# Kernel optimization log

Measured on AMD Instinct MI355X. Metric: run time of the kernel, lower is better.

Reference implementation:

```python
import jax, jax.numpy as jnp
import numpy as np
import math

B, S, E, H = 4, 1024, 1024, 16
DK = E // H  # 64


def setup_inputs() -> dict:
    key = jax.random.key(0)
    ks = jax.random.split(key, 10)
    sc = 0.02
    inp = {
        "x": jax.random.normal(ks[0], (B, S, E), dtype=jnp.float32),
        "mask": jax.random.randint(ks[1], (B, S, S), 0, 2, dtype=jnp.int32),
        "Wq": jax.random.normal(ks[2], (E, E), dtype=jnp.float32) * sc,
        "bq": jnp.zeros((E,), dtype=jnp.float32),
        "Wk": jax.random.normal(ks[3], (E, E), dtype=jnp.float32) * sc,
        "bk": jnp.zeros((E,), dtype=jnp.float32),
        "Wv": jax.random.normal(ks[4], (E, E), dtype=jnp.float32) * sc,
        "bv": jnp.zeros((E,), dtype=jnp.float32),
        "Wo": jax.random.normal(ks[5], (E, E), dtype=jnp.float32) * sc,
        "bo": jnp.zeros((E,), dtype=jnp.float32),
    }
    return inp


def _split_heads(t):
    # [B, S, E] -> [B, H, S, DK]
    return t.reshape(B, S, H, DK).transpose(0, 2, 1, 3)


def reference(x, mask, Wq, bq, Wk, bk, Wv, bv, Wo, bo):
    # Linear projections (torch Linear: y = x @ W.T + b)
    q = _split_heads(x @ Wq.T + bq)
    k = _split_heads(x @ Wk.T + bk)
    v = _split_heads(x @ Wv.T + bv)  # computed but discarded, faithful to source bug
    # scores: [B, H, S, S]
    scores = jnp.einsum('bhqd,bhkd->bhqk', q, k) / jnp.float32(math.sqrt(DK))
    scores = jnp.where(mask[:, None, :, :] == 0, jnp.float32(-1e9), scores)
    scores = jax.nn.softmax(scores, axis=-1)
    # NOTE: source forward keeps dropout(scores) (eval mode -> identity) and
    # DISCARDS matmul(scores, v). We replicate that exactly.
    attn = scores  # [B, H, S, S]
    attn = attn.transpose(0, 2, 1, 3).reshape(B, -1, E)  # [B, S*S/DK, E]
    return attn @ Wo.T + bo
```

## Files before the change

kernel.cpp:

```cpp
#include <hip/hip_runtime.h>

typedef __bf16 bf16;
typedef __attribute__((ext_vector_type(8))) __bf16 bf16x8;
typedef __attribute__((ext_vector_type(4))) float f32x4;


__device__ __forceinline__ unsigned short f2bf(float f) {
    union { float f; unsigned u; } v; v.f = f;
    unsigned r = v.u + 0x7FFFu + ((v.u >> 16) & 1u);
    return (unsigned short)(r >> 16);
}

__device__ __forceinline__ void stage128x64(const bf16* g, int ld_elems,
                                            bf16* lds, int tid) {
    const char* gb = (const char*)g;
    const int ldb = ld_elems * 2;
#pragma unroll
    for (int r = 0; r < 4; ++r) {
        int lin = r * 256 + tid;
        int row = lin >> 3;
        int ch  = (lin & 7) ^ (row & 7);
        __builtin_amdgcn_global_load_lds(
            (const __attribute__((address_space(1))) void*)(gb + (size_t)row * ldb + ch * 16),
            (__attribute__((address_space(3))) void*)(lds + lin * 8),
            16, 0, 0);
    }
}

__device__ __forceinline__ void stage_half512(const bf16* g, bf16* lds, int tid) {
    const char* gb = (const char*)g;
#pragma unroll
    for (int r = 0; r < 2; ++r) {
        int lin = r * 512 + tid;
        int row = lin >> 3;
        int ch  = (lin & 7) ^ (row & 7);
        __builtin_amdgcn_global_load_lds(
            (const __attribute__((address_space(1))) void*)(gb + (size_t)row * 2048 + ch * 16),
            (__attribute__((address_space(3))) void*)(lds + lin * 8),
            16, 0, 0);
    }
}

__device__ __forceinline__ void mma_tile(const bf16* As, const bf16* Bs,
                                         int wm, int wn, int lane,
                                         f32x4 acc[4][4]) {
    const int lm = lane & 15;
    const int g  = lane >> 4;
#pragma unroll
    for (int ks = 0; ks < 2; ++ks) {
        const int c = ks * 4 + g;
        bf16x8 a[4], b[4];
#pragma unroll
        for (int t = 0; t < 4; ++t) {
            const int row = wm * 64 + t * 16 + lm;
            a[t] = *(const bf16x8*)(As + row * 64 + ((c ^ (row & 7)) << 3));
        }
#pragma unroll
        for (int t = 0; t < 4; ++t) {
            const int row = wn * 64 + t * 16 + lm;
            b[t] = *(const bf16x8*)(Bs + row * 64 + ((c ^ (row & 7)) << 3));
        }
#pragma unroll
        for (int i = 0; i < 4; ++i)
#pragma unroll
            for (int j = 0; j < 4; ++j)
                acc[i][j] = __builtin_amdgcn_mfma_f32_16x16x32_bf16(a[i], b[j], acc[i][j], 0, 0, 0);
    }
}


__global__ void convert_kernel(const float* __restrict__ x,  const float* __restrict__ Wq,
                               const float* __restrict__ Wk, const float* __restrict__ Wo,
                               unsigned short* xb, unsigned short* Wqb,
                               unsigned short* Wkb, unsigned short* Wob) {
    size_t i = ((size_t)blockIdx.x * 256 + threadIdx.x) * 4;
    const float* src; unsigned short* dst; size_t off;
    if      (i < 4194304) { src = x;  dst = xb;  off = i; }
    else if (i < 5242880) { src = Wq; dst = Wqb; off = i - 4194304; }
    else if (i < 6291456) { src = Wk; dst = Wkb; off = i - 5242880; }
    else                  { src = Wo; dst = Wob; off = i - 6291456; }
    float4 v = *(const float4*)(src + off);
    ushort4 o;
    o.x = f2bf(v.x); o.y = f2bf(v.y); o.z = f2bf(v.z); o.w = f2bf(v.w);
    *(ushort4*)(dst + off) = o;
}

__global__ __launch_bounds__(256) void proj_kernel(
        const bf16* __restrict__ X, const bf16* __restrict__ Wqb,
        const bf16* __restrict__ Wkb, const float* __restrict__ bq,
        const float* __restrict__ bk, unsigned short* Qb, unsigned short* Kb) {
    __shared__ bf16 As[128 * 64];
    __shared__ bf16 Bs[128 * 64];
    const int tid = threadIdx.x, wid = tid >> 6, lane = tid & 63;
    const int wm = wid >> 1, wn = wid & 1;
    const int n0 = blockIdx.x * 128, m0 = blockIdx.y * 128;
    const bf16*  W    = blockIdx.z ? Wkb : Wqb;
    const float* bias = blockIdx.z ? bk  : bq;
    unsigned short* Out = blockIdx.z ? Kb : Qb;

    f32x4 acc[4][4];
    const f32x4 z4 = {0.f, 0.f, 0.f, 0.f};
#pragma unroll
    for (int i = 0; i < 4; ++i)
#pragma unroll
        for (int j = 0; j < 4; ++j) acc[i][j] = z4;

    for (int kt = 0; kt < 16; ++kt) {
        stage128x64(X + (size_t)m0 * 1024 + kt * 64, 1024, As, tid);
        stage128x64(W + (size_t)n0 * 1024 + kt * 64, 1024, Bs, tid);
        __syncthreads();
        mma_tile(As, Bs, wm, wn, lane, acc);
        __syncthreads();
    }

    const int q = lane >> 4, lm = lane & 15;
#pragma unroll
    for (int j = 0; j < 4; ++j) {
        const int col = n0 + wn * 64 + j * 16 + lm;
        const float bc = bias[col];
#pragma unroll
        for (int i = 0; i < 4; ++i)
#pragma unroll
            for (int r = 0; r < 4; ++r) {
                const int row = m0 + wm * 64 + i * 16 + q * 4 + r;
                Out[(size_t)row * 1024 + col] = f2bf(acc[i][j][r] + bc);
            }
    }
}

__global__ __launch_bounds__(256) void scores_kernel(
        const bf16* __restrict__ Qb, const bf16* __restrict__ Kb,
        const int* __restrict__ mask, unsigned short* Pun, float* Z) {
    __shared__ bf16 As[128 * 64];
    __shared__ bf16 Bs[2][128 * 64];
    __shared__ float Zs[2][128];
    const int tid = threadIdx.x, wid = tid >> 6, lane = tid & 63;
    const int wm = wid >> 1, wn = wid & 1;
    const int i0 = blockIdx.x * 128;
    const int h = blockIdx.y & 15, b = blockIdx.y >> 4;
    const int q = lane >> 4, lm = lane & 15;

    const bf16* Qh = Qb + ((size_t)(b * 1024 + i0)) * 1024 + h * 64;
    const bf16* Kh = Kb + ((size_t)(b * 1024)) * 1024 + h * 64;

    stage128x64(Qh, 1024, As, tid);
    stage128x64(Kh, 1024, Bs[0], tid);

    float rs[4][4];
#pragma unroll
    for (int i = 0; i < 4; ++i)
#pragma unroll
        for (int r = 0; r < 4; ++r) rs[i][r] = 0.f;

    for (int jt = 0; jt < 8; ++jt) {
        __syncthreads();
        if (jt < 7)
            stage128x64(Kh + (size_t)(jt + 1) * 128 * 1024, 1024, Bs[(jt + 1) & 1], tid);

        f32x4 acc[4][4];
        const f32x4 z4 = {0.f, 0.f, 0.f, 0.f};
#pragma unroll
        for (int i = 0; i < 4; ++i)
#pragma unroll
            for (int j = 0; j < 4; ++j) acc[i][j] = z4;
        mma_tile(As, Bs[jt & 1], wm, wn, lane, acc);

#pragma unroll
        for (int i = 0; i < 4; ++i)
#pragma unroll
            for (int r = 0; r < 4; ++r) {
                const int ii = i0 + wm * 64 + i * 16 + q * 4 + r;
                const size_t mrow = (size_t)b * 16384 + (size_t)ii * 16 + h;
#pragma unroll
                for (int j = 0; j < 4; ++j) {
                    const int jj = jt * 128 + wn * 64 + j * 16 + lm;
                    const float s = acc[i][j][r] * 0.125f;
                    const int mk = mask[((size_t)b * 1024 + ii) * 1024 + jj];
                    const float p = mk ? __expf(s) : 0.f;
                    Pun[mrow * 1024 + jj] = f2bf(p);
                    rs[i][r] += p;
                }
            }
    }

#pragma unroll
    for (int i = 0; i < 4; ++i)
#pragma unroll
        for (int r = 0; r < 4; ++r) {
            float v = rs[i][r];
            for (int off = 1; off < 16; off <<= 1) v += __shfl_xor(v, off, 16);
            if (lm == 0) Zs[wn][wm * 64 + i * 16 + q * 4 + r] = v;
        }
    __syncthreads();
    if (tid < 128) {
        const size_t m = (size_t)b * 16384 + (size_t)(i0 + tid) * 16 + h;
        Z[m] = Zs[0][tid] + Zs[1][tid];
    }
}

__global__ __launch_bounds__(512, 2) void out_gemm_kernel(
        const bf16* __restrict__ Pun, const bf16* __restrict__ Wob,
        const float* __restrict__ Z, const float* __restrict__ bo,
        float* __restrict__ out) {
    __shared__ bf16 As[2][2][128 * 64];
    __shared__ bf16 Bs[2][2][128 * 64];
    const int tid = threadIdx.x, wid = tid >> 6, lane = tid & 63;
    const int wm = wid >> 2, wn = wid & 3;
    const int lm = lane & 15, g = lane >> 4;

    const int bx = blockIdx.x, xcd = bx & 7, j = bx >> 3;
    const int m0 = (xcd * 32 + (j >> 2)) * 256;
    const int n0 = (j & 3) * 256;
    const bf16* Apan = Pun + (size_t)m0 * 1024;
    const bf16* Bpan = Wob + (size_t)n0 * 1024;

    f32x4 acc[8][4];
    const f32x4 z4 = {0.f, 0.f, 0.f, 0.f};
#pragma unroll
    for (int mi = 0; mi < 8; ++mi)
#pragma unroll
        for (int nj = 0; nj < 4; ++nj) acc[mi][nj] = z4;

    stage_half512(Bpan,                   Bs[0][0], tid);
    stage_half512(Bpan + 128 * 1024,      Bs[0][1], tid);
    stage_half512(Apan,                   As[0][0], tid);
    stage_half512(Apan + 128 * 1024,      As[0][1], tid);
    stage_half512(Bpan + 64,              Bs[1][0], tid);
    stage_half512(Bpan + 128 * 1024 + 64, Bs[1][1], tid);
    stage_half512(Apan + 64,              As[1][0], tid);
    asm volatile("s_waitcnt vmcnt(6)" ::: "memory");
    __builtin_amdgcn_s_barrier();
    __builtin_amdgcn_sched_barrier(0);

    bf16x8 b[8];

#define MFMA16(MH, KS)                                                        \
    _Pragma("unroll")                                                         \
    for (int mi = 0; mi < 4; ++mi)                                            \
      _Pragma("unroll")                                                       \
      for (int nj = 0; nj < 4; ++nj)                                          \
        acc[(MH) * 4 + mi][nj] = __builtin_amdgcn_mfma_f32_16x16x32_bf16(     \
            a[mi], b[(KS) * 4 + nj], acc[(MH) * 4 + mi][nj], 0, 0, 0);

#define PHASE(BUF, MH, KS, RB, STAGE, GATE)                                   \
  {                                                                           \
    const bf16* pA = &As[BUF][wm][((MH) * 64 + lm) * 64];                     \
    const int csk = (((KS) * 4 + g) ^ (lm & 7)) << 3;                         \
    bf16x8 a[4];                                                              \
    _Pragma("unroll")                                                         \
    for (int mi = 0; mi < 4; ++mi)                                            \
      a[mi] = *(const bf16x8*)(pA + mi * 16 * 64 + csk);                      \
    if (RB) {                                                                 \
      const bf16* pB = &Bs[BUF][wn >> 1][((wn & 1) * 64 + lm) * 64];          \
      _Pragma("unroll")                                                       \
      for (int k2 = 0; k2 < 2; ++k2) {                                        \
        const int cs2 = ((k2 * 4 + g) ^ (lm & 7)) << 3;                       \
        _Pragma("unroll")                                                     \
        for (int nj = 0; nj < 4; ++nj)                                        \
          b[k2 * 4 + nj] = *(const bf16x8*)(pB + nj * 16 * 64 + cs2);         \
      }                                                                       \
    }                                                                         \
    STAGE;                                                                    \
    __builtin_amdgcn_s_barrier();                                             \
    asm volatile("s_waitcnt lgkmcnt(0)" ::: "memory");                        \
    __builtin_amdgcn_sched_barrier(0);                                        \
    __builtin_amdgcn_s_setprio(1);                                            \
    MFMA16(MH, KS);                                                           \
    __builtin_amdgcn_s_setprio(0);                                            \
    __builtin_amdgcn_sched_barrier(0);                                        \
    GATE;                                                                     \
    __builtin_amdgcn_s_barrier();                                             \
    __builtin_amdgcn_sched_barrier(0);                                        \
  }

#pragma unroll 1
    for (int t = 0; t < 16; t += 2) {
        const bool more = (t < 14);
        PHASE(0, 0, 0, true,
              stage_half512(Apan + 128 * 1024 + (t + 1) * 64, As[1][1], tid), )
        PHASE(0, 1, 0, false,
              if (more) { stage_half512(Bpan + (t + 2) * 64, Bs[0][0], tid);
                          stage_half512(Bpan + 128 * 1024 + (t + 2) * 64, Bs[0][1], tid); }, )
        PHASE(0, 0, 1, false, , )
        PHASE(0, 1, 1, false,
              if (more) stage_half512(Apan + (t + 2) * 64, As[0][0], tid),
              if (more) { asm volatile("s_waitcnt vmcnt(6)" ::: "memory"); }
              else      { asm volatile("s_waitcnt vmcnt(0)" ::: "memory"); } )
        PHASE(1, 0, 0, true,
              if (more) stage_half512(Apan + 128 * 1024 + (t + 2) * 64, As[0][1], tid), )
        PHASE(1, 1, 0, false,
              if (more) { stage_half512(Bpan + (t + 3) * 64, Bs[1][0], tid);
                          stage_half512(Bpan + 128 * 1024 + (t + 3) * 64, Bs[1][1], tid); }, )
        PHASE(1, 0, 1, false, , )
        PHASE(1, 1, 1, false,
              if (more) stage_half512(Apan + (t + 3) * 64, As[1][0], tid),
              if (more) { asm volatile("s_waitcnt vmcnt(6)" ::: "memory"); } )
    }
#undef PHASE
#undef MFMA16

#pragma unroll
    for (int mi = 0; mi < 8; ++mi) {
#pragma unroll
        for (int r = 0; r < 4; ++r) {
            const int row = m0 + wm * 128 + mi * 16 + g * 4 + r;
            const float zi = 1.0f / Z[row];
#pragma unroll
            for (int nj = 0; nj < 4; ++nj) {
                const int col = n0 + wn * 64 + nj * 16 + lm;
                out[(size_t)row * 1024 + col] = acc[mi][nj][r] * zi + bo[col];
            }
        }
    }
}


extern "C" void kernel_launch(void* const* d_in, const int* in_sizes, int n_in,
                              void* d_out, int out_size, void* d_ws, size_t ws_size,
                              hipStream_t stream) {
    (void)in_sizes; (void)n_in; (void)out_size; (void)ws_size;
    const float* x    = (const float*)d_in[0];
    const int*   mask = (const int*)d_in[1];
    const float* Wq   = (const float*)d_in[2];
    const float* bq   = (const float*)d_in[3];
    const float* Wk   = (const float*)d_in[4];
    const float* bk   = (const float*)d_in[5];
    const float* Wo   = (const float*)d_in[8];
    const float* bo   = (const float*)d_in[9];

    char* ws = (char*)d_ws;
    bf16*  xb  = (bf16*)(ws);
    bf16*  Wqb = (bf16*)(ws + 8388608);
    bf16*  Wkb = (bf16*)(ws + 10485760);
    bf16*  Wob = (bf16*)(ws + 12582912);
    bf16*  Qb  = (bf16*)(ws + 14680064);
    bf16*  Kb  = (bf16*)(ws + 23068672);
    float* Z   = (float*)(ws + 31457280);
    bf16*  Pun = (bf16*)(ws + 31981568);

    convert_kernel<<<7168, 256, 0, stream>>>(x, Wq, Wk, Wo,
        (unsigned short*)xb, (unsigned short*)Wqb, (unsigned short*)Wkb,
        (unsigned short*)Wob);
    proj_kernel<<<dim3(8, 32, 2), 256, 0, stream>>>(xb, Wqb, Wkb, bq, bk,
        (unsigned short*)Qb, (unsigned short*)Kb);
    scores_kernel<<<dim3(8, 64), 256, 0, stream>>>(Qb, Kb, mask,
        (unsigned short*)Pun, Z);
    out_gemm_kernel<<<1024, 512, 0, stream>>>(Pun, Wob, Z, bo, (float*)d_out);
}
```

Measured before the change: 545.9 us.

## Pack mask into bitwords and stage score tiles in LDS for coalesced stores

Adds a pre-pass that packs the int32 attention mask into 64-bit ballot words, so the scores kernel reads one word per row segment instead of 16 int32 loads per head. This removes the repeated reads of the full mask by each of the 16 heads. The scores kernel now writes exp-probabilities into an LDS tile and then stores them to global memory as 16-byte vectors instead of scattered 2-byte stores. The cost is an extra kernel launch, extra __syncthreads per tile, and reuse of the Wqb workspace region for the packed mask after projection.

```diff
diff --git a/kernel.cpp b/kernel.cpp
--- a/kernel.cpp
+++ b/kernel.cpp
@@ -85,6 +85,13 @@
     *(ushort4*)(dst + off) = o;
 }
 
+__global__ void maskpack_kernel(const int* __restrict__ mask,
+                                unsigned long long* __restrict__ mw) {
+    const int gid = blockIdx.x * 256 + threadIdx.x;
+    const unsigned long long bal = __ballot(mask[gid] != 0);
+    if ((threadIdx.x & 63) == 0) mw[gid >> 6] = bal;
+}
+
 __global__ __launch_bounds__(256) void proj_kernel(
         const bf16* __restrict__ X, const bf16* __restrict__ Wqb,
         const bf16* __restrict__ Wkb, const float* __restrict__ bq,
@@ -130,10 +137,12 @@
 
 __global__ __launch_bounds__(256) void scores_kernel(
         const bf16* __restrict__ Qb, const bf16* __restrict__ Kb,
-        const int* __restrict__ mask, unsigned short* Pun, float* Z) {
+        const unsigned long long* __restrict__ maskw,
+        unsigned short* Pun, float* Z) {
     __shared__ bf16 As[128 * 64];
     __shared__ bf16 Bs[2][128 * 64];
-    __shared__ float Zs[2][128];
+    __shared__ __align__(16) unsigned short Pl[2][64][128];
+    float (*Zs)[128] = (float (*)[128])(&Pl[0][0][0]);
     const int tid = threadIdx.x, wid = tid >> 6, lane = tid & 63;
     const int wm = wid >> 1, wn = wid & 1;
     const int i0 = blockIdx.x * 128;
@@ -166,21 +175,39 @@
         mma_tile(As, Bs[jt & 1], wm, wn, lane, acc);
 
 #pragma unroll
-        for (int i = 0; i < 4; ++i)
-#pragma unroll
-            for (int r = 0; r < 4; ++r) {
-                const int ii = i0 + wm * 64 + i * 16 + q * 4 + r;
-                const size_t mrow = (size_t)b * 16384 + (size_t)ii * 16 + h;
-#pragma unroll
-                for (int j = 0; j < 4; ++j) {
-                    const int jj = jt * 128 + wn * 64 + j * 16 + lm;
-                    const float s = acc[i][j][r] * 0.125f;
-                    const int mk = mask[((size_t)b * 1024 + ii) * 1024 + jj];
-                    const float p = mk ? __expf(s) : 0.f;
-                    Pun[mrow * 1024 + jj] = f2bf(p);
-                    rs[i][r] += p;
-                }
+        for (int half = 0; half < 2; ++half) {
+            if (wm == half) {
+#pragma unroll
+                for (int i = 0; i < 4; ++i)
+#pragma unroll
+                    for (int r = 0; r < 4; ++r) {
+                        const int lrow = i * 16 + q * 4 + r;
+                        const int ii = i0 + half * 64 + lrow;
+                        const unsigned long long W =
+                            maskw[(size_t)(b * 1024 + ii) * 16 + jt * 2 + wn];
+                        const unsigned lo = (unsigned)W, hi = (unsigned)(W >> 32);
+#pragma unroll
+                        for (int j = 0; j < 4; ++j) {
+                            const unsigned mb =
+                                (((j & 2) ? hi : lo) >> (((j & 1) << 4) + lm)) & 1u;
+                            const float s = acc[i][j][r] * 0.125f;
+                            const float p = mb ? __expf(s) : 0.f;
+                            rs[i][r] += p;
+                            Pl[half][lrow][wn * 64 + j * 16 + lm] = f2bf(p);
+                        }
+                    }
             }
+            __syncthreads();
+#pragma unroll
+            for (int pass = 0; pass < 4; ++pass) {
+                const int chunk = pass * 256 + tid;
+                const int row = chunk >> 4, c16 = chunk & 15;
+                const size_t mrow =
+                    (size_t)b * 16384 + (size_t)(i0 + half * 64 + row) * 16 + h;
+                *(bf16x8*)(Pun + mrow * 1024 + jt * 128 + c16 * 8) =
+                    *(const bf16x8*)(&Pl[half][row][c16 * 8]);
+            }
+        }
     }
 
 #pragma unroll
@@ -337,13 +364,15 @@
     bf16*  Kb  = (bf16*)(ws + 23068672);
     float* Z   = (float*)(ws + 31457280);
     bf16*  Pun = (bf16*)(ws + 31981568);
+    unsigned long long* maskw = (unsigned long long*)(ws + 8388608);
 
     convert_kernel<<<7168, 256, 0, stream>>>(x, Wq, Wk, Wo,
         (unsigned short*)xb, (unsigned short*)Wqb, (unsigned short*)Wkb,
         (unsigned short*)Wob);
     proj_kernel<<<dim3(8, 32, 2), 256, 0, stream>>>(xb, Wqb, Wkb, bq, bk,
         (unsigned short*)Qb, (unsigned short*)Kb);
-    scores_kernel<<<dim3(8, 64), 256, 0, stream>>>(Qb, Kb, mask,
+    maskpack_kernel<<<16384, 256, 0, stream>>>(mask, maskw);
+    scores_kernel<<<dim3(8, 64), 256, 0, stream>>>(Qb, Kb, maskw,
         (unsigned short*)Pun, Z);
     out_gemm_kernel<<<1024, 512, 0, stream>>>(Pun, Wob, Z, bo, (float*)d_out);
 }
```

Result: faster. 524.0 us (-4.0%).
